# Performance work log

Measured on AMD Instinct MI355X. Metric: run time of the kernel, lower is better.

The kernel has to match this reference:

```python
import jax, jax.numpy as jnp
import numpy as np

N_HEAD = 32
N_KV = 8
D = 2048
HD = D // N_HEAD
FF = 8192
EPS = 1e-5
THETA = 10000.0


def rms_norm(x, g):
    return g * x / jnp.sqrt(jnp.mean(x * x, axis=-1, keepdims=True) + EPS)


def rope(x):
    # x: [B, H, T, hd]; lucidrains interleaved RoPE
    T = x.shape[2]
    inv_freq = 1.0 / (THETA ** (jnp.arange(0, HD, 2, dtype=jnp.float32) / HD))  # [hd/2]
    freqs = jnp.arange(T, dtype=jnp.float32)[:, None] * inv_freq[None, :]       # [T, hd/2]
    freqs = jnp.repeat(freqs, 2, axis=-1)                                        # [T, hd]
    cos, sin = jnp.cos(freqs), jnp.sin(freqs)
    x1 = x[..., ::2]
    x2 = x[..., 1::2]
    rot = jnp.stack([-x2, x1], axis=-1).reshape(x.shape)
    return x * cos + rot * sin


def attention(x, wq, wk, wv, wo):
    B, T, C = x.shape
    q = (x @ wq).reshape(B, T, N_HEAD, HD).transpose(0, 2, 1, 3)  # [B,H,T,hd]
    k = (x @ wk).reshape(B, T, N_KV, HD).transpose(0, 2, 1, 3)    # [B,Hkv,T,hd]
    v = (x @ wv).reshape(B, T, N_KV, HD).transpose(0, 2, 1, 3)
    q = rope(q)
    k = rope(k)
    rep = N_HEAD // N_KV
    k = jnp.repeat(k, rep, axis=1)
    v = jnp.repeat(v, rep, axis=1)
    att = jnp.einsum('bhqd,bhkd->bhqk', q, k) * (1.0 / np.sqrt(HD))
    causal = jnp.tril(jnp.ones((T, T), dtype=bool))
    att = jnp.where(causal[None, None], att, -jnp.inf)
    att = jax.nn.softmax(att, axis=-1)
    y = jnp.einsum('bhqk,bhkd->bhqd', att, v)
    y = y.transpose(0, 2, 1, 3).reshape(B, T, C)
    return y @ wo


def mlp(x, wg, wu, wd):
    return (jax.nn.silu(x @ wg) * (x @ wu)) @ wd


def setup_inputs() -> dict:
    key = jax.random.key(0)
    ks = jax.random.split(key, 9)
    s = lambda fan_in: 1.0 / np.sqrt(fan_in)
    return {
        'x': jax.random.normal(ks[0], (1, 2048, D), dtype=jnp.float32),
        'g1': jnp.ones((D,), dtype=jnp.float32),
        'wq': jax.random.normal(ks[1], (D, D), dtype=jnp.float32) * s(D),
        'wk': jax.random.normal(ks[2], (D, N_KV * HD), dtype=jnp.float32) * s(D),
        'wv': jax.random.normal(ks[3], (D, N_KV * HD), dtype=jnp.float32) * s(D),
        'wo': jax.random.normal(ks[4], (D, D), dtype=jnp.float32) * s(D),
        'g2': jnp.ones((D,), dtype=jnp.float32),
        'wg': jax.random.normal(ks[5], (D, FF), dtype=jnp.float32) * s(D),
        'wu': jax.random.normal(ks[6], (D, FF), dtype=jnp.float32) * s(D),
        'wd': jax.random.normal(ks[7], (FF, D), dtype=jnp.float32) * s(FF),
    }


def reference(x, g1, wq, wk, wv, wo, g2, wg, wu, wd):
    residual = x
    x = rms_norm(x, g1)
    x = x + attention(x, wq, wk, wv, wo)
    x = rms_norm(x, g2)
    x = x + mlp(x, wg, wu, wd)
    x = x + residual
    return x
```

## Files before the change

kernel.cpp:

```cpp
#include <hip/hip_runtime.h>
#include <cstdint>
#include <cstddef>


typedef __attribute__((ext_vector_type(8))) short short8;
typedef __attribute__((ext_vector_type(4))) float f32x4;
typedef __attribute__((ext_vector_type(16))) float f32x16;

typedef __attribute__((address_space(1))) const void gvoid_t;
typedef __attribute__((address_space(3))) void lvoid_t;

__device__ inline unsigned short f2b(float f) {
  unsigned int u = __float_as_uint(f);
  u += 0x7fffu + ((u >> 16) & 1u);
  return (unsigned short)(u >> 16);
}
__device__ inline float b2f(unsigned short s) {
  return __uint_as_float((unsigned int)s << 16);
}
__device__ inline unsigned int pkbf(float lo, float hi) {
  unsigned int r;
  asm("v_cvt_pk_bf16_f32 %0, %1, %2" : "=v"(r) : "v"(lo), "v"(hi));
  return r;
}

__device__ inline void xcd_part(int& bx, int& by) {
  const int nbx = gridDim.x, nby = gridDim.y;
  const int cpx = nbx >> 3;
  const int f = by * nbx + bx;
  const int xcd = f & 7;
  const int t = f >> 3;
  bx = xcd * cpx + t / nby;
  by = t % nby;
}

__global__ __launch_bounds__(256) void transpose_cast(
    const float* __restrict__ W, unsigned short* __restrict__ Wt,
    int R, int ldW) {
  __shared__ unsigned short s[32 * 36];
  const int r0 = blockIdx.y * 32, c0 = blockIdx.x * 32;
  const int tr = threadIdx.x >> 3, tc = (threadIdx.x & 7) << 2;
  const float4 v = *(const float4*)(W + (size_t)(r0 + tr) * ldW + c0 + tc);
  s[tr * 36 + tc + 0] = f2b(v.x);
  s[tr * 36 + tc + 1] = f2b(v.y);
  s[tr * 36 + tc + 2] = f2b(v.z);
  s[tr * 36 + tc + 3] = f2b(v.w);
  __syncthreads();
  ushort4 o;
  o.x = s[(tc + 0) * 36 + tr];
  o.y = s[(tc + 1) * 36 + tr];
  o.z = s[(tc + 2) * 36 + tr];
  o.w = s[(tc + 3) * 36 + tr];
  *(ushort4*)(Wt + (size_t)(c0 + tr) * R + r0 + tc) = o;
}

__global__ __launch_bounds__(256) void rmsnorm(
    const float* __restrict__ X, const float* __restrict__ g,
    unsigned short* __restrict__ ob) {
  const int row = blockIdx.x;
  const float* x = X + (size_t)row * 2048;
  float ss = 0.f;
  for (int i = threadIdx.x; i < 2048; i += 256) { float v = x[i]; ss += v * v; }
  for (int off = 32; off; off >>= 1) ss += __shfl_down(ss, off, 64);
  __shared__ float red[4];
  if ((threadIdx.x & 63) == 0) red[threadIdx.x >> 6] = ss;
  __syncthreads();
  const float tot = red[0] + red[1] + red[2] + red[3];
  const float r = rsqrtf(tot * (1.f / 2048.f) + 1e-5f);
  for (int i = threadIdx.x; i < 2048; i += 256)
    ob[(size_t)row * 2048 + i] = f2b(x[i] * g[i] * r);
}

__global__ __launch_bounds__(256) void add_res(
    const unsigned short* __restrict__ h2, const float* __restrict__ x,
    float* __restrict__ out) {
  const int i = blockIdx.x * 256 + threadIdx.x;
  const ushort4 h = ((const ushort4*)h2)[i];
  const float4 xv = ((const float4*)x)[i];
  float4 o;
  o.x = xv.x + b2f(h.x); o.y = xv.y + b2f(h.y);
  o.z = xv.z + b2f(h.z); o.w = xv.w + b2f(h.w);
  ((float4*)out)[i] = o;
}

__global__ __launch_bounds__(256) void prefill_b2f(
    const unsigned short* __restrict__ h, float* __restrict__ out) {
  const int i = blockIdx.x * 256 + threadIdx.x;
  const ushort4 v = ((const ushort4*)h)[i];
  float4 o;
  o.x = b2f(v.x); o.y = b2f(v.y); o.z = b2f(v.z); o.w = b2f(v.w);
  ((float4*)out)[i] = o;
}

__global__ __launch_bounds__(256, 2) void gemm_bt(
    const unsigned short* __restrict__ A, const unsigned short* __restrict__ Bt,
    float* Cf, unsigned short* Cb,
    const unsigned short* add1b, const float* add2,
    int N, int Kfull, int Kchunk, int epi, int Tld,
    unsigned short* Cb2, unsigned short* Cb3) {
  __shared__ unsigned short As[128 * 64];
  __shared__ unsigned short Bs[128 * 64];
  const int tid = threadIdx.x;
  const int wave = tid >> 6, lane = tid & 63;
  const int quad = lane >> 4, l16 = lane & 15;
  int bx = blockIdx.x, by = blockIdx.y;
  xcd_part(bx, by);
  const int m0 = by * 128, n0 = bx * 128;
  const int wr = (wave >> 1) * 64, wc = (wave & 1) * 64;
  const int Ks = blockIdx.z * Kchunk, Ke = Ks + Kchunk;

  f32x4 acc[4][4] = {};

  for (int k0 = Ks; k0 < Ke; k0 += 64) {
#pragma unroll
    for (int p = 0; p < 4; ++p) {
      const int idx = p * 256 + tid;
      const int row = idx >> 3;
      const int kc = ((idx & 7) ^ (row & 7)) * 8;
      const unsigned short* gA = A + (size_t)(m0 + row) * Kfull + k0 + kc;
      const unsigned short* gB = Bt + (size_t)(n0 + row) * Kfull + k0 + kc;
      unsigned short* lA = As + (size_t)(p * 256 + wave * 64) * 8;
      unsigned short* lB = Bs + (size_t)(p * 256 + wave * 64) * 8;
      __builtin_amdgcn_global_load_lds((gvoid_t*)gA, (lvoid_t*)lA, 16, 0, 0);
      __builtin_amdgcn_global_load_lds((gvoid_t*)gB, (lvoid_t*)lB, 16, 0, 0);
    }
    __syncthreads();

#pragma unroll
    for (int ks = 0; ks < 2; ++ks) {
      short8 af[4], bf[4];
#pragma unroll
      for (int i = 0; i < 4; ++i) {
        const int row = wr + i * 16 + l16;
        af[i] = *(const short8*)(As + row * 64 +
                                 (((ks << 2) | quad) ^ (row & 7)) * 8);
      }
#pragma unroll
      for (int j = 0; j < 4; ++j) {
        const int row = wc + j * 16 + l16;
        bf[j] = *(const short8*)(Bs + row * 64 +
                                 (((ks << 2) | quad) ^ (row & 7)) * 8);
      }
#pragma unroll
      for (int i = 0; i < 4; ++i)
#pragma unroll
        for (int j = 0; j < 4; ++j)
          acc[i][j] = __builtin_amdgcn_mfma_f32_16x16x32_bf16(
              af[i], bf[j], acc[i][j], 0, 0, 0);
    }
    __syncthreads();
  }

  if (epi == 7 && n0 >= 2560) {
#pragma unroll
    for (int i = 0; i < 4; ++i)
#pragma unroll
      for (int j = 0; j < 4; ++j) {
        const int row = m0 + wr + i * 16 + quad * 4;
        const int col = n0 + wc + j * 16 + l16 - 2560;
        ushort4 o;
        o.x = f2b(acc[i][j][0]); o.y = f2b(acc[i][j][1]);
        o.z = f2b(acc[i][j][2]); o.w = f2b(acc[i][j][3]);
        *(ushort4*)(Cb3 + (size_t)col * Tld + row) = o;
      }
    return;
  }

#pragma unroll
  for (int i = 0; i < 4; ++i)
#pragma unroll
    for (int j = 0; j < 4; ++j) {
      const int rowb = m0 + wr + i * 16 + quad * 4;
      const int col = n0 + wc + j * 16 + l16;
      float invf = 0.f, sgn = 0.f;
      if (epi == 7) {
        const int ip = (col & 63) >> 1;
        invf = __expf(-(float)ip * 0.28782313662f);
        sgn = (col & 1) ? 1.f : -1.f;
      }
#pragma unroll
      for (int r = 0; r < 4; ++r) {
        const size_t idx = (size_t)(rowb + r) * N + col;
        const float v = acc[i][j][r];
        const float p = __shfl_xor(v, 1, 64);
        if (epi == 1) {
          Cf[idx] = v + b2f(add1b[idx]);
        } else if (epi == 8) {
          atomicAdd(&Cf[idx], v);
        } else {
          float sn, cs;
          __sincosf((float)(rowb + r) * invf, &sn, &cs);
          const unsigned short o = f2b(v * cs + sgn * p * sn);
          if (col < 2048)
            Cb[(size_t)(rowb + r) * 2048 + col] = o;
          else
            Cb2[(size_t)(rowb + r) * 512 + col - 2048] = o;
        }
      }
    }
}

__global__ __launch_bounds__(256, 2) void gemm_gu(
    const unsigned short* __restrict__ A, const unsigned short* __restrict__ Bg,
    const unsigned short* __restrict__ Bu, unsigned short* __restrict__ act,
    int N, int K) {
  __shared__ unsigned short As[128 * 64];
  __shared__ unsigned short Gs[128 * 64];
  __shared__ unsigned short Us[128 * 64];
  const int tid = threadIdx.x;
  const int wave = tid >> 6, lane = tid & 63;
  const int quad = lane >> 4, l16 = lane & 15;
  int bx = blockIdx.x, by = blockIdx.y;
  xcd_part(bx, by);
  const int m0 = by * 128, n0 = bx * 128;
  const int wr = (wave >> 1) * 64, wc = (wave & 1) * 64;

  f32x4 aG[4][4] = {}, aU[4][4] = {};

  for (int k0 = 0; k0 < K; k0 += 64) {
#pragma unroll
    for (int p = 0; p < 4; ++p) {
      const int idx = p * 256 + tid;
      const int row = idx >> 3;
      const int kc = ((idx & 7) ^ (row & 7)) * 8;
      const size_t off = (size_t)(p * 256 + wave * 64) * 8;
      __builtin_amdgcn_global_load_lds(
          (gvoid_t*)(A + (size_t)(m0 + row) * K + k0 + kc),
          (lvoid_t*)(As + off), 16, 0, 0);
      __builtin_amdgcn_global_load_lds(
          (gvoid_t*)(Bg + (size_t)(n0 + row) * K + k0 + kc),
          (lvoid_t*)(Gs + off), 16, 0, 0);
      __builtin_amdgcn_global_load_lds(
          (gvoid_t*)(Bu + (size_t)(n0 + row) * K + k0 + kc),
          (lvoid_t*)(Us + off), 16, 0, 0);
    }
    __syncthreads();

#pragma unroll
    for (int ks = 0; ks < 2; ++ks) {
      short8 af[4], bg[4], bu[4];
#pragma unroll
      for (int i = 0; i < 4; ++i) {
        const int row = wr + i * 16 + l16;
        af[i] = *(const short8*)(As + row * 64 +
                                 (((ks << 2) | quad) ^ (row & 7)) * 8);
      }
#pragma unroll
      for (int j = 0; j < 4; ++j) {
        const int row = wc + j * 16 + l16;
        const int kk = (((ks << 2) | quad) ^ (row & 7)) * 8;
        bg[j] = *(const short8*)(Gs + row * 64 + kk);
        bu[j] = *(const short8*)(Us + row * 64 + kk);
      }
#pragma unroll
      for (int i = 0; i < 4; ++i)
#pragma unroll
        for (int j = 0; j < 4; ++j) {
          aG[i][j] = __builtin_amdgcn_mfma_f32_16x16x32_bf16(
              af[i], bg[j], aG[i][j], 0, 0, 0);
          aU[i][j] = __builtin_amdgcn_mfma_f32_16x16x32_bf16(
              af[i], bu[j], aU[i][j], 0, 0, 0);
        }
    }
    __syncthreads();
  }

#pragma unroll
  for (int i = 0; i < 4; ++i)
#pragma unroll
    for (int j = 0; j < 4; ++j) {
      const int rowb = m0 + wr + i * 16 + quad * 4;
      const int col = n0 + wc + j * 16 + l16;
#pragma unroll
      for (int r = 0; r < 4; ++r) {
        const float g = aG[i][j][r], u = aU[i][j][r];
        act[(size_t)(rowb + r) * N + col] = f2b(g / (1.f + __expf(-g)) * u);
      }
    }
}

__global__ __launch_bounds__(256) void flash_attn(
    const unsigned short* __restrict__ Qb, const unsigned short* __restrict__ Kb,
    const unsigned short* __restrict__ Vt, unsigned short* __restrict__ Y,
    int T) {
  const int tid = threadIdx.x;
  const int wave = tid >> 6, lane = tid & 63;
  const int l32 = lane & 31, hi = lane >> 5;
  const int h = blockIdx.y, kvh = h >> 2;
  const int qt = (blockIdx.x + wave * 16) << 5;
  const int qrow = qt + l32;

  short8 qf[4];
#pragma unroll
  for (int ds = 0; ds < 4; ++ds) {
    short8 v = *(const short8*)(Qb + (size_t)qrow * 2048 + h * 64 +
                                ds * 16 + hi * 8);
#pragma unroll
    for (int e = 0; e < 8; ++e)
      v[e] = (short)f2b(b2f((unsigned short)v[e]) * 0.125f);
    qf[ds] = v;
  }

  const unsigned short* Kp = Kb + (size_t)l32 * 512 + kvh * 64 + hi * 8;
  const unsigned short* Vp = Vt + (size_t)(kvh * 64 + l32) * T + hi * 8;

  const int niter = (qt >> 5) + 1;
  float m_i = -3e38f, l_i = 0.f;
  f32x16 o0 = {}, o1 = {};

  short8 kf[4], kfn[4];
#pragma unroll
  for (int ds = 0; ds < 4; ++ds) kf[ds] = *(const short8*)(Kp + ds * 16);

  for (int it = 0; it < niter; ++it) {
    const int k0 = it << 5;
    short8 vf[2][2];
#pragma unroll
    for (int dt = 0; dt < 2; ++dt)
#pragma unroll
      for (int ks = 0; ks < 2; ++ks)
        vf[dt][ks] =
            *(const short8*)(Vp + (size_t)dt * 32 * T + k0 + ks * 16);
    const int kn = (k0 + 32 < 2016) ? k0 + 32 : 2016;
#pragma unroll
    for (int ds = 0; ds < 4; ++ds)
      kfn[ds] = *(const short8*)(Kp + (size_t)kn * 512 + ds * 16);

    f32x16 S = {};
#pragma unroll
    for (int ds = 0; ds < 4; ++ds)
      S = __builtin_amdgcn_mfma_f32_32x32x16_bf16(kf[ds], qf[ds], S, 0, 0, 0);

    float s[16];
#pragma unroll
    for (int r = 0; r < 16; ++r) s[r] = S[r];
    if (k0 == qt) {
#pragma unroll
      for (int r = 0; r < 16; ++r)
        if (((r & 3) + 8 * (r >> 2) + 4 * hi) > l32) s[r] = -3e38f;
    }

    float tmax = s[0];
#pragma unroll
    for (int r = 1; r < 16; ++r) tmax = fmaxf(tmax, s[r]);
    tmax = fmaxf(tmax, __shfl_xor(tmax, 32, 64));

    if (!__all(tmax <= m_i + 8.f)) {
      const float mn = fmaxf(m_i, tmax);
      const float al = __expf(m_i - mn);
#pragma unroll
      for (int r = 0; r < 16; ++r) { o0[r] *= al; o1[r] *= al; }
      l_i *= al;
      m_i = mn;
    }

    float p[16], rs = 0.f;
#pragma unroll
    for (int r = 0; r < 16; ++r) { p[r] = __expf(s[r] - m_i); rs += p[r]; }
    rs += __shfl_xor(rs, 32, 64);
    l_i += rs;

    short8 pf[2];
#pragma unroll
    for (int ks = 0; ks < 2; ++ks) {
      const int rb = ks * 8;
      const unsigned int a0 = pkbf(p[rb + 0], p[rb + 1]);
      const unsigned int a1 = pkbf(p[rb + 2], p[rb + 3]);
      const unsigned int b0 = pkbf(p[rb + 4], p[rb + 5]);
      const unsigned int b1 = pkbf(p[rb + 6], p[rb + 7]);
      const unsigned int t0 = __shfl_xor((int)(hi ? a0 : b0), 32, 64);
      const unsigned int t1 = __shfl_xor((int)(hi ? a1 : b1), 32, 64);
      union { unsigned int u[4]; short8 v; } pu;
      pu.u[0] = hi ? t0 : a0;
      pu.u[1] = hi ? t1 : a1;
      pu.u[2] = hi ? b0 : t0;
      pu.u[3] = hi ? b1 : t1;
      pf[ks] = pu.v;
    }

#pragma unroll
    for (int ks = 0; ks < 2; ++ks) {
      o0 = __builtin_amdgcn_mfma_f32_32x32x16_bf16(vf[0][ks], pf[ks], o0,
                                                   0, 0, 0);
      o1 = __builtin_amdgcn_mfma_f32_32x32x16_bf16(vf[1][ks], pf[ks], o1,
                                                   0, 0, 0);
    }
#pragma unroll
    for (int ds = 0; ds < 4; ++ds) kf[ds] = kfn[ds];
  }

  const float inv = 1.f / l_i;
  unsigned short* Yp = Y + (size_t)qrow * 2048 + h * 64 + hi * 4;
#pragma unroll
  for (int g = 0; g < 4; ++g) {
    ushort4 u0, u1;
    u0.x = f2b(o0[g * 4 + 0] * inv); u0.y = f2b(o0[g * 4 + 1] * inv);
    u0.z = f2b(o0[g * 4 + 2] * inv); u0.w = f2b(o0[g * 4 + 3] * inv);
    *(ushort4*)(Yp + g * 8) = u0;
    u1.x = f2b(o1[g * 4 + 0] * inv); u1.y = f2b(o1[g * 4 + 1] * inv);
    u1.z = f2b(o1[g * 4 + 2] * inv); u1.w = f2b(o1[g * 4 + 3] * inv);
    *(ushort4*)(Yp + 32 + g * 8) = u1;
  }
}

extern "C" void kernel_launch(void* const* d_in, const int* in_sizes, int n_in,
                              void* d_out, int out_size, void* d_ws,
                              size_t ws_size, hipStream_t stream) {
  const float* x  = (const float*)d_in[0];
  const float* g1 = (const float*)d_in[1];
  const float* wq = (const float*)d_in[2];
  const float* wk = (const float*)d_in[3];
  const float* wv = (const float*)d_in[4];
  const float* wo = (const float*)d_in[5];
  const float* g2 = (const float*)d_in[6];
  const float* wg = (const float*)d_in[7];
  const float* wu = (const float*)d_in[8];
  const float* wd = (const float*)d_in[9];
  float* out = (float*)d_out;

  const int T = 2048, Dm = 2048, FF = 8192;
  char* ws = (char*)d_ws;
  const size_t MB = (size_t)1 << 20;

  unsigned short* wq_t = (unsigned short*)(ws + 0 * MB);
  unsigned short* wk_t = (unsigned short*)(ws + 8 * MB);
  unsigned short* wv_t = (unsigned short*)(ws + 10 * MB);
  unsigned short* wo_t = (unsigned short*)(ws + 12 * MB);
  unsigned short* wg_t = (unsigned short*)(ws + 20 * MB);
  unsigned short* wu_t = (unsigned short*)(ws + 52 * MB);
  unsigned short* h1_b = (unsigned short*)(ws + 84 * MB);
  unsigned short* h2_b = (unsigned short*)(ws + 92 * MB);
  float*          x2_f = (float*)(ws + 100 * MB);
  unsigned short* gate = (unsigned short*)(ws + 100 * MB);
  unsigned short* q_b  = (unsigned short*)(ws + 132 * MB);
  unsigned short* k_b  = (unsigned short*)(ws + 140 * MB);
  unsigned short* vt_b = (unsigned short*)(ws + 142 * MB);
  unsigned short* y_b  = (unsigned short*)(ws + 144 * MB);
  unsigned short* wd_t = (unsigned short*)(ws + 132 * MB);

  transpose_cast<<<dim3(64, 64), 256, 0, stream>>>(wq, wq_t, Dm, Dm);
  transpose_cast<<<dim3(16, 64), 256, 0, stream>>>(wk, wk_t, Dm, 512);
  transpose_cast<<<dim3(16, 64), 256, 0, stream>>>(wv, wv_t, Dm, 512);
  transpose_cast<<<dim3(64, 64), 256, 0, stream>>>(wo, wo_t, Dm, Dm);
  transpose_cast<<<dim3(256, 64), 256, 0, stream>>>(wg, wg_t, Dm, FF);
  transpose_cast<<<dim3(256, 64), 256, 0, stream>>>(wu, wu_t, Dm, FF);

  rmsnorm<<<T, 256, 0, stream>>>(x, g1, h1_b);

  gemm_bt<<<dim3(24, 16), 256, 0, stream>>>(h1_b, wq_t, nullptr, q_b, nullptr,
                                            nullptr, 3072, Dm, Dm, 7, T, k_b,
                                            vt_b);

  flash_attn<<<dim3(16, 32), 256, 0, stream>>>(q_b, k_b, vt_b, y_b, T);

  prefill_b2f<<<(T * Dm / 4) / 256, 256, 0, stream>>>(h1_b, x2_f);
  gemm_bt<<<dim3(16, 16, 2), 256, 0, stream>>>(y_b, wo_t, x2_f, nullptr,
                                               nullptr, nullptr, Dm, Dm,
                                               Dm / 2, 8, 0, nullptr, nullptr);

  transpose_cast<<<dim3(64, 256), 256, 0, stream>>>(wd, wd_t, FF, Dm);

  rmsnorm<<<T, 256, 0, stream>>>(x2_f, g2, h2_b);

  gemm_gu<<<dim3(64, 16), 256, 0, stream>>>(h2_b, wg_t, wu_t, gate, FF, Dm);

  add_res<<<(T * Dm / 4) / 256, 256, 0, stream>>>(h2_b, x, out);
  gemm_bt<<<dim3(16, 16, 2), 256, 0, stream>>>(gate, wd_t, out, nullptr,
                                               nullptr, nullptr, Dm, FF,
                                               FF / 2, 8, 0, nullptr, nullptr);
}
```

Measured before the change: 702.3 us.

## Fuse residual prefill into rmsnorm, batch transposes, table RoPE, deepen split-K

Merges the prefill_b2f and add_res elementwise passes into the rmsnorm kernel, so one kernel now writes both the bf16 normalized output and the fp32 residual-seeded accumulator. Pairs of weight transpose launches are merged via a z grid dimension. RoPE cos/sin values come from a precomputed table instead of per-element sincos in the QKV GEMM epilogue. The down-projection split-K grows from 2 to 4, which raises parallelism but doubles the atomic adds into the output. The RoPE table lives at the h2_b workspace offset, which is safe only because it is consumed before h2_b is written.

```diff
diff --git a/kernel.cpp b/kernel.cpp
--- a/kernel.cpp
+++ b/kernel.cpp
@@ -36,11 +36,14 @@
 
 __global__ __launch_bounds__(256) void transpose_cast(
     const float* __restrict__ W, unsigned short* __restrict__ Wt,
+    const float* __restrict__ W2, unsigned short* __restrict__ Wt2,
     int R, int ldW) {
   __shared__ unsigned short s[32 * 36];
+  const float* Ws = blockIdx.z ? W2 : W;
+  unsigned short* Wd = blockIdx.z ? Wt2 : Wt;
   const int r0 = blockIdx.y * 32, c0 = blockIdx.x * 32;
   const int tr = threadIdx.x >> 3, tc = (threadIdx.x & 7) << 2;
-  const float4 v = *(const float4*)(W + (size_t)(r0 + tr) * ldW + c0 + tc);
+  const float4 v = *(const float4*)(Ws + (size_t)(r0 + tr) * ldW + c0 + tc);
   s[tr * 36 + tc + 0] = f2b(v.x);
   s[tr * 36 + tc + 1] = f2b(v.y);
   s[tr * 36 + tc + 2] = f2b(v.z);
@@ -51,12 +54,22 @@
   o.y = s[(tc + 1) * 36 + tr];
   o.z = s[(tc + 2) * 36 + tr];
   o.w = s[(tc + 3) * 36 + tr];
-  *(ushort4*)(Wt + (size_t)(c0 + tr) * R + r0 + tc) = o;
-}
-
-__global__ __launch_bounds__(256) void rmsnorm(
+  *(ushort4*)(Wd + (size_t)(c0 + tr) * R + r0 + tc) = o;
+}
+
+__global__ __launch_bounds__(256) void rope_fill(float2* __restrict__ tab) {
+  const int idx = blockIdx.x * 256 + threadIdx.x;
+  const int t = idx >> 5, ip = idx & 31;
+  const float invf = __expf(-(float)ip * 0.28782313662f);
+  float sn, cs;
+  __sincosf((float)t * invf, &sn, &cs);
+  tab[idx] = make_float2(cs, sn);
+}
+
+__global__ __launch_bounds__(256) void rmsnorm2(
     const float* __restrict__ X, const float* __restrict__ g,
-    unsigned short* __restrict__ ob) {
+    unsigned short* __restrict__ ob, float* __restrict__ of,
+    const float* __restrict__ xadd) {
   const int row = blockIdx.x;
   const float* x = X + (size_t)row * 2048;
   float ss = 0.f;
@@ -67,35 +80,19 @@
   __syncthreads();
   const float tot = red[0] + red[1] + red[2] + red[3];
   const float r = rsqrtf(tot * (1.f / 2048.f) + 1e-5f);
-  for (int i = threadIdx.x; i < 2048; i += 256)
-    ob[(size_t)row * 2048 + i] = f2b(x[i] * g[i] * r);
-}
-
-__global__ __launch_bounds__(256) void add_res(
-    const unsigned short* __restrict__ h2, const float* __restrict__ x,
-    float* __restrict__ out) {
-  const int i = blockIdx.x * 256 + threadIdx.x;
-  const ushort4 h = ((const ushort4*)h2)[i];
-  const float4 xv = ((const float4*)x)[i];
-  float4 o;
-  o.x = xv.x + b2f(h.x); o.y = xv.y + b2f(h.y);
-  o.z = xv.z + b2f(h.z); o.w = xv.w + b2f(h.w);
-  ((float4*)out)[i] = o;
-}
-
-__global__ __launch_bounds__(256) void prefill_b2f(
-    const unsigned short* __restrict__ h, float* __restrict__ out) {
-  const int i = blockIdx.x * 256 + threadIdx.x;
-  const ushort4 v = ((const ushort4*)h)[i];
-  float4 o;
-  o.x = b2f(v.x); o.y = b2f(v.y); o.z = b2f(v.z); o.w = b2f(v.w);
-  ((float4*)out)[i] = o;
+  const size_t base = (size_t)row * 2048;
+  for (int i = threadIdx.x; i < 2048; i += 256) {
+    const unsigned short ush = f2b(x[i] * g[i] * r);
+    ob[base + i] = ush;
+    const float add = xadd ? xadd[base + i] : 0.f;
+    of[base + i] = add + b2f(ush);
+  }
 }
 
 __global__ __launch_bounds__(256, 2) void gemm_bt(
     const unsigned short* __restrict__ A, const unsigned short* __restrict__ Bt,
     float* Cf, unsigned short* Cb,
-    const unsigned short* add1b, const float* add2,
+    const float2* __restrict__ rope, const float* add2,
     int N, int Kfull, int Kchunk, int epi, int Tld,
     unsigned short* Cb2, unsigned short* Cb3) {
   __shared__ unsigned short As[128 * 64];
@@ -172,25 +169,18 @@
     for (int j = 0; j < 4; ++j) {
       const int rowb = m0 + wr + i * 16 + quad * 4;
       const int col = n0 + wc + j * 16 + l16;
-      float invf = 0.f, sgn = 0.f;
-      if (epi == 7) {
-        const int ip = (col & 63) >> 1;
-        invf = __expf(-(float)ip * 0.28782313662f);
-        sgn = (col & 1) ? 1.f : -1.f;
-      }
+      const int ip = (col & 63) >> 1;
+      const float sgn = (col & 1) ? 1.f : -1.f;
 #pragma unroll
       for (int r = 0; r < 4; ++r) {
         const size_t idx = (size_t)(rowb + r) * N + col;
         const float v = acc[i][j][r];
         const float p = __shfl_xor(v, 1, 64);
-        if (epi == 1) {
-          Cf[idx] = v + b2f(add1b[idx]);
-        } else if (epi == 8) {
+        if (epi == 8) {
           atomicAdd(&Cf[idx], v);
         } else {
-          float sn, cs;
-          __sincosf((float)(rowb + r) * invf, &sn, &cs);
-          const unsigned short o = f2b(v * cs + sgn * p * sn);
+          const float2 cssn = rope[(rowb + r) * 32 + ip];
+          const unsigned short o = f2b(v * cssn.x + sgn * p * cssn.y);
           if (col < 2048)
             Cb[(size_t)(rowb + r) * 2048 + col] = o;
           else
@@ -430,6 +420,7 @@
   unsigned short* wu_t = (unsigned short*)(ws + 52 * MB);
   unsigned short* h1_b = (unsigned short*)(ws + 84 * MB);
   unsigned short* h2_b = (unsigned short*)(ws + 92 * MB);
+  float2*        ropet = (float2*)(ws + 92 * MB);
   float*          x2_f = (float*)(ws + 100 * MB);
   unsigned short* gate = (unsigned short*)(ws + 100 * MB);
   unsigned short* q_b  = (unsigned short*)(ws + 132 * MB);
@@ -438,34 +429,36 @@
   unsigned short* y_b  = (unsigned short*)(ws + 144 * MB);
   unsigned short* wd_t = (unsigned short*)(ws + 132 * MB);
 
-  transpose_cast<<<dim3(64, 64), 256, 0, stream>>>(wq, wq_t, Dm, Dm);
-  transpose_cast<<<dim3(16, 64), 256, 0, stream>>>(wk, wk_t, Dm, 512);
-  transpose_cast<<<dim3(16, 64), 256, 0, stream>>>(wv, wv_t, Dm, 512);
-  transpose_cast<<<dim3(64, 64), 256, 0, stream>>>(wo, wo_t, Dm, Dm);
-  transpose_cast<<<dim3(256, 64), 256, 0, stream>>>(wg, wg_t, Dm, FF);
-  transpose_cast<<<dim3(256, 64), 256, 0, stream>>>(wu, wu_t, Dm, FF);
-
-  rmsnorm<<<T, 256, 0, stream>>>(x, g1, h1_b);
-
-  gemm_bt<<<dim3(24, 16), 256, 0, stream>>>(h1_b, wq_t, nullptr, q_b, nullptr,
+  rope_fill<<<256, 256, 0, stream>>>(ropet);
+  transpose_cast<<<dim3(64, 64), 256, 0, stream>>>(wq, wq_t, nullptr, nullptr,
+                                                   Dm, Dm);
+  transpose_cast<<<dim3(16, 64, 2), 256, 0, stream>>>(wk, wk_t, wv, wv_t,
+                                                      Dm, 512);
+  transpose_cast<<<dim3(64, 64), 256, 0, stream>>>(wo, wo_t, nullptr, nullptr,
+                                                   Dm, Dm);
+  transpose_cast<<<dim3(256, 64, 2), 256, 0, stream>>>(wg, wg_t, wu, wu_t,
+                                                       Dm, FF);
+
+  rmsnorm2<<<T, 256, 0, stream>>>(x, g1, h1_b, x2_f, nullptr);
+
+  gemm_bt<<<dim3(24, 16), 256, 0, stream>>>(h1_b, wq_t, nullptr, q_b, ropet,
                                             nullptr, 3072, Dm, Dm, 7, T, k_b,
                                             vt_b);
 
   flash_attn<<<dim3(16, 32), 256, 0, stream>>>(q_b, k_b, vt_b, y_b, T);
 
-  prefill_b2f<<<(T * Dm / 4) / 256, 256, 0, stream>>>(h1_b, x2_f);
   gemm_bt<<<dim3(16, 16, 2), 256, 0, stream>>>(y_b, wo_t, x2_f, nullptr,
                                                nullptr, nullptr, Dm, Dm,
                                                Dm / 2, 8, 0, nullptr, nullptr);
 
-  transpose_cast<<<dim3(64, 256), 256, 0, stream>>>(wd, wd_t, FF, Dm);
-
-  rmsnorm<<<T, 256, 0, stream>>>(x2_f, g2, h2_b);
+  transpose_cast<<<dim3(64, 256), 256, 0, stream>>>(wd, wd_t, nullptr, nullptr,
+                                                    FF, Dm);
+
+  rmsnorm2<<<T, 256, 0, stream>>>(x2_f, g2, h2_b, out, x);
 
   gemm_gu<<<dim3(64, 16), 256, 0, stream>>>(h2_b, wg_t, wu_t, gate, FF, Dm);
 
-  add_res<<<(T * Dm / 4) / 256, 256, 0, stream>>>(h2_b, x, out);
-  gemm_bt<<<dim3(16, 16, 2), 256, 0, stream>>>(gate, wd_t, out, nullptr,
+  gemm_bt<<<dim3(16, 16, 4), 256, 0, stream>>>(gate, wd_t, out, nullptr,
                                                nullptr, nullptr, Dm, FF,
-                                               FF / 2, 8, 0, nullptr, nullptr);
-}
+                                               FF / 4, 8, 0, nullptr, nullptr);
+}
```

Result: no change. 710.5 us (+1.2%).
